# Kernel tuning notes

Measured on AMD Instinct MI355X. Metric: run time of the kernel, lower is better.

The kernel has to match this reference:

```python
import jax, jax.numpy as jnp
import numpy as np
import math

B, S, H, NH = 2, 2048, 1024, 16
DH = H // NH  # head_dim = 64


def setup_inputs() -> dict:
    key = jax.random.key(0)
    k1, k2, k3 = jax.random.split(key, 3)
    hidden_states = jax.random.normal(k1, (B, S, H), dtype=jnp.float32)
    # causal additive mask: 0 on/below diagonal, large negative above
    causal = jnp.tril(jnp.ones((S, S), dtype=jnp.float32))
    attention_mask = jnp.where(causal == 1, 0.0, -1e9).astype(jnp.float32)
    attention_mask = jnp.broadcast_to(attention_mask[None, None], (B, 1, S, S))
    w_qkv = jax.random.normal(k2, (H, 3 * H), dtype=jnp.float32) * (H ** -0.5)
    w_out = jax.random.normal(k3, (H, H), dtype=jnp.float32) * (H ** -0.5)
    return {"hidden_states": hidden_states, "attention_mask": attention_mask,
            "w_qkv": w_qkv, "w_out": w_out}


def reference(hidden_states, attention_mask, w_qkv, w_out):
    # fused QKV projection (bias-free Linear)
    qkv = hidden_states @ w_qkv                       # [B,S,3H]
    qkv = qkv.reshape(B, S, 3, NH, DH)
    qkv = jnp.transpose(qkv, (2, 0, 3, 1, 4))         # [3,B,NH,S,DH]
    q, k, v = qkv[0], qkv[1], qkv[2]
    scores = jnp.einsum('bhqd,bhkd->bhqk', q, k) / math.sqrt(DH)
    scores = scores + attention_mask                  # [B,NH,S,S]
    probs = jax.nn.softmax(scores, axis=-1)
    ctx = jnp.einsum('bhqk,bhkd->bhqd', probs, v)     # [B,NH,S,DH]
    ctx = jnp.transpose(ctx, (0, 2, 1, 3)).reshape(B, S, H)
    return ctx @ w_out                                # [B,S,H]
```

## Files before the change

### kernel.cpp

```cpp
#include <hip/hip_runtime.h>

#define S_LEN 2048
#define NHEAD 16
#define DHEAD 64
#define HDIM  1024
#define BATCH 2
#define MTOK  (BATCH * S_LEN)

using bf16x8 = __bf16 __attribute__((ext_vector_type(8)));
using f32x4  = float __attribute__((ext_vector_type(4)));
using f32x16 = float __attribute__((ext_vector_type(16)));
using u16x4  = unsigned short __attribute__((ext_vector_type(4)));
using u32x4a = unsigned __attribute__((ext_vector_type(4)));

typedef unsigned short ushort_t;

static __device__ __forceinline__ ushort_t f2bf(float f) {
  union { float f; unsigned u; } v{f};
  unsigned r = v.u + 0x7FFFu + ((v.u >> 16) & 1u);
  return (ushort_t)(r >> 16);
}

static __device__ __forceinline__ unsigned pkbf(float a, float b) {
  return ((unsigned)f2bf(b) << 16) | (unsigned)f2bf(a);
}

static __device__ __forceinline__ unsigned cvtpk(float a, float b) {
  unsigned r;
  asm("v_cvt_pk_bf16_f32 %0, %1, %2" : "=v"(r) : "v"(a), "v"(b));
  return r;
}

static __device__ __forceinline__ bf16x8 mk8(unsigned a, unsigned b, unsigned c, unsigned d) {
  u32x4a t = {a, b, c, d};
  return __builtin_bit_cast(bf16x8, t);
}

static __device__ __forceinline__ void gload_lds16(const void* g, void* lds) {
  __builtin_amdgcn_global_load_lds(
      (const __attribute__((address_space(1))) void*)g,
      (__attribute__((address_space(3))) void*)lds, 16, 0, 0);
}

static __device__ __forceinline__ float bpermf(int paddr, float v) {
  return __builtin_bit_cast(float,
      __builtin_amdgcn_ds_bpermute(paddr, __builtin_bit_cast(int, v)));
}
static __device__ __forceinline__ unsigned bpermu(int paddr, unsigned v) {
  return (unsigned)__builtin_amdgcn_ds_bpermute(paddr, (int)v);
}

__global__ __launch_bounds__(256) void cast_bf16(const float* __restrict__ in,
                                                 ushort_t* __restrict__ out, int n4) {
  int i = blockIdx.x * blockDim.x + threadIdx.x;
  if (i >= n4) return;
  float4 v = *((const float4*)in + i);
  u16x4 o = { f2bf(v.x), f2bf(v.y), f2bf(v.z), f2bf(v.w) };
  *((u16x4*)out + i) = o;
}

__global__ void transpose_cast(const float* __restrict__ in, ushort_t* __restrict__ out,
                               int R, int C) {
  __shared__ float tile[32][33];
  int bx = blockIdx.x, by = blockIdx.y;
  int tx = threadIdx.x, ty = threadIdx.y;
  #pragma unroll
  for (int i = 0; i < 32; i += 8)
    tile[ty + i][tx] = in[(size_t)(by * 32 + ty + i) * C + bx * 32 + tx];
  __syncthreads();
  #pragma unroll
  for (int i = 0; i < 32; i += 8)
    out[(size_t)(bx * 32 + ty + i) * R + by * 32 + tx] = f2bf(tile[tx][ty + i]);
}

__global__ __launch_bounds__(256) void gemm_bt128(
    const ushort_t* __restrict__ A, const ushort_t* __restrict__ Bt,
    int M, int N, int K, int mode,
    ushort_t* __restrict__ outQ, ushort_t* __restrict__ outK, ushort_t* __restrict__ outV,
    float* __restrict__ outF) {
  __shared__ __align__(16) ushort_t lA[128 * 32];
  __shared__ __align__(16) ushort_t lB[128 * 32];
  const int bm = blockIdx.x, bn = blockIdx.y;
  const int tid = threadIdx.x;
  const int wv = tid >> 6, lane = tid & 63;
  const int wm = wv >> 1, wn = wv & 1;
  const int lo = lane & 15, hi = lane >> 4;

  f32x4 acc[4][4] = {};

  const ushort_t* gA = A + (size_t)(bm * 128 + wv * 32 + (lane >> 2)) * K + (lane & 3) * 8;
  const ushort_t* gB = Bt + (size_t)(bn * 128 + wv * 32 + (lane >> 2)) * K + (lane & 3) * 8;
  char* lAb = (char*)lA + wv * 2048;
  char* lBb = (char*)lB + wv * 2048;

  for (int kk = 0; kk < K; kk += 32) {
    __syncthreads();
    gload_lds16(gA + kk,           lAb);
    gload_lds16(gA + kk + 16 * K,  lAb + 1024);
    gload_lds16(gB + kk,           lBb);
    gload_lds16(gB + kk + 16 * K,  lBb + 1024);
    __syncthreads();
    bf16x8 af[4], bfr[4];
    #pragma unroll
    for (int i = 0; i < 4; ++i)
      af[i] = *(const bf16x8*)&lA[(wm * 64 + i * 16 + lo) * 32 + hi * 8];
    #pragma unroll
    for (int j = 0; j < 4; ++j)
      bfr[j] = *(const bf16x8*)&lB[(wn * 64 + j * 16 + lo) * 32 + hi * 8];
    #pragma unroll
    for (int i = 0; i < 4; ++i)
      #pragma unroll
      for (int j = 0; j < 4; ++j)
        acc[i][j] = __builtin_amdgcn_mfma_f32_16x16x32_bf16(af[i], bfr[j], acc[i][j], 0, 0, 0);
  }

  #pragma unroll
  for (int i = 0; i < 4; ++i) {
    #pragma unroll
    for (int j = 0; j < 4; ++j) {
      #pragma unroll
      for (int r = 0; r < 4; ++r) {
        int gm = bm * 128 + wm * 64 + i * 16 + hi * 4 + r;
        int gn = bn * 128 + wn * 64 + j * 16 + lo;
        float v = acc[i][j][r];
        if (mode == 0) {
          int which = gn >> 10;
          int h = (gn >> 6) & 15;
          int d = gn & 63;
          int b = gm >> 11;
          int s = gm & 2047;
          size_t hb = (size_t)(b * NHEAD + h) * (S_LEN * DHEAD);
          if (which == 0) {
            size_t addr = hb + (size_t)((s >> 5) * 2048 +
                          ((d >> 4) * 2 + ((d >> 3) & 1)) * 256 + (s & 31) * 8 + (d & 7));
            outQ[addr] = f2bf(v * 0.18033688011112042f);
          } else if (which == 1) {
            size_t addr = hb + (size_t)((s >> 6) * 4096 + ((s >> 5) & 1) * 2048 +
                          ((d >> 4) * 2 + ((d >> 3) & 1)) * 256 + (s & 31) * 8 + (d & 7));
            outK[addr] = f2bf(v);
          } else {
            size_t addr = hb + (size_t)((s >> 6) * 4096 + (d >> 5) * 2048 +
                          (((s >> 4) & 3) * 2 + ((s >> 3) & 1)) * 256 + (d & 31) * 8 + (s & 7));
            outV[addr] = f2bf(v);
          }
        } else {
          outF[(size_t)gm * N + gn] = v;
        }
      }
    }
  }
}

__global__ __launch_bounds__(512, 2) void attn_sw(
    const ushort_t* __restrict__ Qb, const ushort_t* __restrict__ Kb,
    const ushort_t* __restrict__ Vt, ushort_t* __restrict__ ctx) {
  const int bid = blockIdx.x;
  const int head = (bid & 7) * 4 + (bid >> 7);
  const int b16 = (bid >> 3) & 15;
  const int tid = threadIdx.x;
  const int wv = tid >> 6, lane = tid & 63;
  const int l31 = lane & 31, hi2 = lane >> 5;

  __shared__ float ldsAcc[4][32][64];
  __shared__ float ldsL[4][64];

  const int sj = (wv < 4) ? wv : ((wv & 3) ^ 2);
  const int st = (sj == 0) ? 2 * b16 : (sj == 1) ? 2 * b16 + 1
               : (sj == 2) ? 63 - 2 * b16 : 62 - 2 * b16;
  const int qbase = st * 32;
  const int qg = qbase + l31;
  const int nbb = (qbase >> 6) + 1;
  const int nh = nbb >> 1;
  const int jb0 = (wv < 4) ? 0 : nh;
  const int jb1 = (wv < 4) ? nh : nbb;
  const int paddr = (lane ^ 32) << 2;

  const size_t hbase = (size_t)head * (S_LEN * DHEAD);
  const ushort_t* vtb = Vt + hbase;

  bf16x8 qf[4];
  {
    const ushort_t* qp = Qb + hbase + st * 2048 + lane * 8;
    #pragma unroll
    for (int si = 0; si < 4; ++si) qf[si] = *(const bf16x8*)(qp + si * 512);
  }

  f32x16 accO[2] = {};
  float l = 0.f;

  auto loadK = [&](bf16x8 (&kf)[2][4], int kvb) {
    const ushort_t* kp = Kb + hbase + (size_t)(kvb >> 6) * 4096 + lane * 8;
    #pragma unroll
    for (int t = 0; t < 2; ++t)
      #pragma unroll
      for (int si = 0; si < 4; ++si)
        kf[t][si] = *(const bf16x8*)(kp + t * 2048 + si * 512);
  };

  auto body = [&](bf16x8 (&kf)[2][4], bf16x8 (&kfn)[2][4], int jb) {
    const int kvb = jb * 64;

    bf16x8 va[2][4];
    {
      const ushort_t* vp = vtb + (size_t)jb * 4096 + lane * 8;
      #pragma unroll
      for (int dt = 0; dt < 2; ++dt)
        #pragma unroll
        for (int ks = 0; ks < 4; ++ks)
          va[dt][ks] = *(const bf16x8*)(vp + dt * 2048 + ks * 512);
    }

    if (jb + 1 < jb1) loadK(kfn, kvb + 64);

    f32x16 p[2];
    #pragma unroll
    for (int t = 0; t < 2; ++t) {
      f32x16 acc = {};
      #pragma unroll
      for (int si = 0; si < 4; ++si)
        acc = __builtin_amdgcn_mfma_f32_32x32x16_bf16(kf[t][si], qf[si], acc, 0, 0, 0);
      p[t] = acc;
    }

    if (jb == nbb - 1) {
      #pragma unroll
      for (int r = 0; r < 16; ++r) {
        int kvq = kvb + ((r & 3) + 8 * (r >> 2) + 4 * hi2);
        if (kvq > qg) p[0][r] = -1e30f;
        if (kvq + 32 > qg) p[1][r] = -1e30f;
      }
    }

    #pragma unroll
    for (int t = 0; t < 2; ++t)
      #pragma unroll
      for (int r = 0; r < 16; ++r) p[t][r] = exp2f(p[t][r] - 24.0f);

    float s16[16];
    #pragma unroll
    for (int r = 0; r < 16; ++r) s16[r] = p[0][r] + p[1][r];
    float s8[8];
    #pragma unroll
    for (int r = 0; r < 8; ++r) s8[r] = s16[r] + s16[r + 8];
    float s4[4];
    #pragma unroll
    for (int r = 0; r < 4; ++r) s4[r] = s8[r] + s8[r + 4];
    float rs = (s4[0] + s4[1]) + (s4[2] + s4[3]);
    rs += bpermf(paddr, rs);
    l += rs;

    bf16x8 PB[4];
    #pragma unroll
    for (int ks = 0; ks < 4; ++ks) {
      const int t = ks >> 1, r0 = (ks & 1) * 8;
      unsigned w0 = cvtpk(p[t][r0 + 0], p[t][r0 + 1]);
      unsigned w1 = cvtpk(p[t][r0 + 2], p[t][r0 + 3]);
      unsigned w2 = cvtpk(p[t][r0 + 4], p[t][r0 + 5]);
      unsigned w3 = cvtpk(p[t][r0 + 6], p[t][r0 + 7]);
      unsigned pw0 = bpermu(paddr, w0), pw1 = bpermu(paddr, w1);
      unsigned pw2 = bpermu(paddr, w2), pw3 = bpermu(paddr, w3);
      unsigned f0 = hi2 ? pw2 : w0;
      unsigned f1 = hi2 ? pw3 : w1;
      unsigned f2 = hi2 ? w2 : pw0;
      unsigned f3 = hi2 ? w3 : pw1;
      PB[ks] = mk8(f0, f1, f2, f3);
    }

    #pragma unroll
    for (int dt = 0; dt < 2; ++dt)
      #pragma unroll
      for (int ks = 0; ks < 4; ++ks)
        accO[dt] = __builtin_amdgcn_mfma_f32_32x32x16_bf16(va[dt][ks], PB[ks], accO[dt], 0, 0, 0);
  };

  bf16x8 kfA[2][4], kfB[2][4];
  if (jb0 < jb1) {
    loadK(kfA, jb0 * 64);
    for (int jb = jb0; jb < jb1; jb += 2) {
      body(kfA, kfB, jb);
      if (jb + 1 < jb1) body(kfB, kfA, jb + 1);
    }
  }

  if (wv >= 4) {
    #pragma unroll
    for (int dt = 0; dt < 2; ++dt)
      #pragma unroll
      for (int r = 0; r < 16; ++r)
        ldsAcc[sj][dt * 16 + r][lane] = accO[dt][r];
    ldsL[sj][lane] = l;
  }
  __syncthreads();
  if (wv < 4) {
    #pragma unroll
    for (int dt = 0; dt < 2; ++dt)
      #pragma unroll
      for (int r = 0; r < 16; ++r)
        accO[dt][r] += ldsAcc[sj][dt * 16 + r][lane];
    l += ldsL[sj][lane];

    const int b = head >> 4, h = head & 15;
    const float inv = 1.0f / l;
    ushort_t* crow = ctx + ((size_t)b * S_LEN + qg) * HDIM + h * 64;
    #pragma unroll
    for (int dt = 0; dt < 2; ++dt)
      #pragma unroll
      for (int g = 0; g < 4; ++g) {
        unsigned w0 = pkbf(accO[dt][g * 4 + 0] * inv, accO[dt][g * 4 + 1] * inv);
        unsigned w1 = pkbf(accO[dt][g * 4 + 2] * inv, accO[dt][g * 4 + 3] * inv);
        unsigned long long wl = ((unsigned long long)w1 << 32) | w0;
        *(unsigned long long*)(crow + dt * 32 + g * 8 + hi2 * 4) = wl;
      }
  }
}

extern "C" void kernel_launch(void* const* d_in, const int* in_sizes, int n_in,
                              void* d_out, int out_size, void* d_ws, size_t ws_size,
                              hipStream_t stream) {
  const float* hs   = (const float*)d_in[0];
  const float* wqkv = (const float*)d_in[2];
  const float* wout = (const float*)d_in[3];
  float* out = (float*)d_out;

  char* ws = (char*)d_ws;
  ushort_t* h_bf   = (ushort_t*)(ws + 0);
  ushort_t* wqkv_t = (ushort_t*)(ws + 8388608);
  ushort_t* wout_t = (ushort_t*)(ws + 14680064);
  ushort_t* Qb     = (ushort_t*)(ws + 16777216);
  ushort_t* Kbuf   = (ushort_t*)(ws + 25165824);
  ushort_t* Vtb    = (ushort_t*)(ws + 33554432);
  ushort_t* ctxb   = (ushort_t*)(ws + 41943040);

  cast_bf16<<<dim3(4096), dim3(256), 0, stream>>>(hs, h_bf, MTOK * HDIM / 4);
  transpose_cast<<<dim3(96, 32), dim3(32, 8), 0, stream>>>(wqkv, wqkv_t, HDIM, 3 * HDIM);
  transpose_cast<<<dim3(32, 32), dim3(32, 8), 0, stream>>>(wout, wout_t, HDIM, HDIM);

  gemm_bt128<<<dim3(32, 24), dim3(256), 0, stream>>>(h_bf, wqkv_t, MTOK, 3 * HDIM, HDIM, 0,
                                                     Qb, Kbuf, Vtb, nullptr);
  attn_sw<<<dim3(512), dim3(512), 0, stream>>>(Qb, Kbuf, Vtb, ctxb);
  gemm_bt128<<<dim3(32, 8), dim3(256), 0, stream>>>(ctxb, wout_t, MTOK, HDIM, HDIM, 1,
                                                    nullptr, nullptr, nullptr, out);
}
```

Before: 130.5 us.

## Double-buffer GEMM LDS tiles with K=64, XOR swizzle, and workgroup remapping

Rewrites the bf16 GEMM main loop to use two LDS buffers with 64-wide K tiles. The next tile is prefetched while the current one is being multiplied, which replaces the two full barriers per iteration with a vmcnt wait and one barrier pair. LDS columns are XOR-swizzled to avoid bank conflicts, and the 1D grid is remapped so neighbouring workgroups spread across XCDs. It also raises MFMA wave priority and sets launch bounds for 2 blocks per CU. The cost is 64 KB of LDS per block, which can limit occupancy.

After: 131.3 us. Within noise of the previous version (+0.6%).

```diff
diff --git a/kernel.cpp b/kernel.cpp
--- a/kernel.cpp
+++ b/kernel.cpp
@@ -73,14 +73,17 @@
     out[(size_t)(bx * 32 + ty + i) * R + by * 32 + tx] = f2bf(tile[tx][ty + i]);
 }
 
-__global__ __launch_bounds__(256) void gemm_bt128(
+__global__ __launch_bounds__(256, 2) void gemm_2ph(
     const ushort_t* __restrict__ A, const ushort_t* __restrict__ Bt,
     int M, int N, int K, int mode,
     ushort_t* __restrict__ outQ, ushort_t* __restrict__ outK, ushort_t* __restrict__ outV,
     float* __restrict__ outF) {
-  __shared__ __align__(16) ushort_t lA[128 * 32];
-  __shared__ __align__(16) ushort_t lB[128 * 32];
-  const int bm = blockIdx.x, bn = blockIdx.y;
+  __shared__ __align__(16) ushort_t lA[2][128 * 64];
+  __shared__ __align__(16) ushort_t lB[2][128 * 64];
+  const int wg = blockIdx.x;
+  const int q8 = (int)(gridDim.x >> 3);
+  const int swz = (wg & 7) * q8 + (wg >> 3);
+  const int bm = swz & 31, bn = swz >> 5;
   const int tid = threadIdx.x;
   const int wv = tid >> 6, lane = tid & 63;
   const int wm = wv >> 1, wn = wv & 1;
@@ -88,30 +91,63 @@
 
   f32x4 acc[4][4] = {};
 
-  const ushort_t* gA = A + (size_t)(bm * 128 + wv * 32 + (lane >> 2)) * K + (lane & 3) * 8;
-  const ushort_t* gB = Bt + (size_t)(bn * 128 + wv * 32 + (lane >> 2)) * K + (lane & 3) * 8;
-  char* lAb = (char*)lA + wv * 2048;
-  char* lBb = (char*)lB + wv * 2048;
-
-  for (int kk = 0; kk < K; kk += 32) {
-    __syncthreads();
-    gload_lds16(gA + kk,           lAb);
-    gload_lds16(gA + kk + 16 * K,  lAb + 1024);
-    gload_lds16(gB + kk,           lBb);
-    gload_lds16(gB + kk + 16 * K,  lBb + 1024);
-    __syncthreads();
-    bf16x8 af[4], bfr[4];
-    #pragma unroll
-    for (int i = 0; i < 4; ++i)
-      af[i] = *(const bf16x8*)&lA[(wm * 64 + i * 16 + lo) * 32 + hi * 8];
-    #pragma unroll
-    for (int j = 0; j < 4; ++j)
-      bfr[j] = *(const bf16x8*)&lB[(wn * 64 + j * 16 + lo) * 32 + hi * 8];
-    #pragma unroll
-    for (int i = 0; i < 4; ++i)
-      #pragma unroll
-      for (int j = 0; j < 4; ++j)
-        acc[i][j] = __builtin_amdgcn_mfma_f32_16x16x32_bf16(af[i], bfr[j], acc[i][j], 0, 0, 0);
+  const int srow = lane >> 3;
+  const int schunk = (lane & 7) ^ srow;
+  const ushort_t* gA = A + (size_t)(bm * 128 + wv * 32 + srow) * K + schunk * 8;
+  const ushort_t* gB = Bt + (size_t)(bn * 128 + wv * 32 + srow) * K + schunk * 8;
+  const int NT = K >> 6;
+
+  auto stage = [&](int t) {
+    const int cur = t & 1;
+    char* da = (char*)&lA[cur][0] + wv * 4096 + lane * 16;
+    char* db = (char*)&lB[cur][0] + wv * 4096 + lane * 16;
+    const ushort_t* sa = gA + t * 64;
+    const ushort_t* sb = gB + t * 64;
+    #pragma unroll
+    for (int i = 0; i < 4; ++i) {
+      gload_lds16(sa + (size_t)i * 8 * K, da + i * 1024);
+      gload_lds16(sb + (size_t)i * 8 * K, db + i * 1024);
+    }
+  };
+
+  stage(0);
+  for (int t = 0; t < NT; ++t) {
+    const int cur = t & 1;
+    if (t + 1 < NT) {
+      stage(t + 1);
+      asm volatile("s_waitcnt vmcnt(8)" ::: "memory");
+    } else {
+      asm volatile("s_waitcnt vmcnt(0)" ::: "memory");
+    }
+    __builtin_amdgcn_s_barrier();
+    __builtin_amdgcn_sched_barrier(0);
+    const ushort_t* pa = &lA[cur][0];
+    const ushort_t* pb = &lB[cur][0];
+    #pragma unroll
+    for (int ks = 0; ks < 2; ++ks) {
+      bf16x8 af[4], bfr[4];
+      #pragma unroll
+      for (int i = 0; i < 4; ++i) {
+        int r = wm * 64 + i * 16 + lo;
+        int c = (ks * 4 + hi) ^ (lo & 7);
+        af[i] = *(const bf16x8*)&pa[r * 64 + c * 8];
+      }
+      #pragma unroll
+      for (int j = 0; j < 4; ++j) {
+        int r = wn * 64 + j * 16 + lo;
+        int c = (ks * 4 + hi) ^ (lo & 7);
+        bfr[j] = *(const bf16x8*)&pb[r * 64 + c * 8];
+      }
+      __builtin_amdgcn_s_setprio(1);
+      #pragma unroll
+      for (int i = 0; i < 4; ++i)
+        #pragma unroll
+        for (int j = 0; j < 4; ++j)
+          acc[i][j] = __builtin_amdgcn_mfma_f32_16x16x32_bf16(af[i], bfr[j], acc[i][j], 0, 0, 0);
+      __builtin_amdgcn_s_setprio(0);
+    }
+    __builtin_amdgcn_sched_barrier(0);
+    __builtin_amdgcn_s_barrier();
   }
 
   #pragma unroll
@@ -335,9 +371,9 @@
   transpose_cast<<<dim3(96, 32), dim3(32, 8), 0, stream>>>(wqkv, wqkv_t, HDIM, 3 * HDIM);
   transpose_cast<<<dim3(32, 32), dim3(32, 8), 0, stream>>>(wout, wout_t, HDIM, HDIM);
 
-  gemm_bt128<<<dim3(32, 24), dim3(256), 0, stream>>>(h_bf, wqkv_t, MTOK, 3 * HDIM, HDIM, 0,
-                                                     Qb, Kbuf, Vtb, nullptr);
+  gemm_2ph<<<dim3(768), dim3(256), 0, stream>>>(h_bf, wqkv_t, MTOK, 3 * HDIM, HDIM, 0,
+                                                Qb, Kbuf, Vtb, nullptr);
   attn_sw<<<dim3(512), dim3(512), 0, stream>>>(Qb, Kbuf, Vtb, ctxb);
-  gemm_bt128<<<dim3(32, 8), dim3(256), 0, stream>>>(ctxb, wout_t, MTOK, HDIM, HDIM, 1,
-                                                    nullptr, nullptr, nullptr, out);
-}
+  gemm_2ph<<<dim3(256), dim3(256), 0, stream>>>(ctxb, wout_t, MTOK, HDIM, HDIM, 1,
+                                                nullptr, nullptr, nullptr, out);
+}
```
